# Optimization experiments

Measured on AMD Instinct MI355X. Metric: run time of the kernel, lower is better.

Reference implementation:

```python
import jax, jax.numpy as jnp
import numpy as np

B, N, C, H = 8, 1024, 768, 12
WBITS, ABITS, PGABITS = 8, 8, 4
TH = 0.99  # greater-than mask threshold on MSB softmax


def quant(x, bits):
    """Fixed-point quantize to `bits` bits, straight-through estimator."""
    step = 2.0 ** (1 - bits)
    q = jnp.round(x / step) * step
    return x + jax.lax.stop_gradient(q - x)


def setup_inputs() -> dict:
    key = jax.random.key(0)
    k1, k2, k3 = jax.random.split(key, 3)
    x = jax.random.normal(k1, (B, N, C), jnp.float32)
    # qkv: QLinear(dim, 3*dim, bias=False); proj: QLinear(dim, dim, bias=True)
    w_qkv = jax.random.normal(k2, (3 * C, C), jnp.float32) * (C ** -0.5)
    w_proj = jax.random.normal(k3, (C, C), jnp.float32) * (C ** -0.5)
    b_proj = jnp.zeros((C,), jnp.float32)
    return {"x": x, "w_qkv": w_qkv, "w_proj": w_proj, "b_proj": b_proj}


def reference(x, w_qkv, w_proj, b_proj):
    d = C // H
    scale = d ** -0.5
    # QLinear: quantize activations and weights, then matmul (no qkv bias)
    qkv = quant(x, ABITS) @ quant(w_qkv, WBITS).T            # [B,N,3C]
    qkv = qkv.reshape(B, N, 3, H, d).transpose(2, 0, 3, 1, 4)  # [3,B,H,N,d]
    qkv = quant(qkv, ABITS)
    q, k, v = qkv[0], qkv[1], qkv[2]
    # low-precision MSB pass
    q_msb = quant(q, PGABITS)
    k_msb = quant(k, PGABITS)
    attn_msb = jax.nn.softmax(
        jnp.einsum('bhqd,bhkd->bhqk', q_msb, k_msb) * scale, axis=-1)
    # GreaterThan with straight-through backward (identity grad)
    gt = (attn_msb > TH).astype(attn_msb.dtype)
    mask = attn_msb + jax.lax.stop_gradient(gt - attn_msb)
    # full-precision pass, masked pre-softmax
    attn = jnp.einsum('bhqd,bhkd->bhqk', q, k) * scale * mask
    attn = quant(jax.nn.softmax(attn, axis=-1), ABITS)
    out = jnp.einsum('bhqk,bhkd->bhqd', attn, v)             # [B,H,N,d]
    out = out.transpose(0, 2, 1, 3).reshape(B, N, C)
    return quant(out, ABITS) @ quant(w_proj, WBITS).T + b_proj
```

## Files before the change

kernel.cpp:

```cpp
#include <hip/hip_runtime.h>

#define NB 8
#define NSEQ 1024
#define NC 768
#define NH 12
#define ND 64
#define NM 8192

typedef _Float16 v8h __attribute__((ext_vector_type(8)));
typedef float v4f __attribute__((ext_vector_type(4)));
typedef int   v4i __attribute__((ext_vector_type(4)));

__device__ __forceinline__ float q8f(float x){ return rintf(x*128.f)*0.0078125f; }
__device__ __forceinline__ int imax2(int a, int b){ return a > b ? a : b; }
__device__ __forceinline__ int imin2(int a, int b){ return a < b ? a : b; }

__device__ __forceinline__ int swz(int r, int g){ return (r<<6) + (((g ^ (r & 7)) & 7)<<3); }

__device__ __forceinline__ void async_cp16(const void* g, void* l) {
  __builtin_amdgcn_global_load_lds(
      (const __attribute__((address_space(1))) unsigned int*)g,
      (__attribute__((address_space(3))) unsigned int*)l, 16, 0, 0);
}

__global__ __launch_bounds__(256) void k_pre(const float* __restrict__ x,
                                             const float* __restrict__ wq,
                                             const float* __restrict__ bias,
                                             _Float16* __restrict__ xt,
                                             _Float16* __restrict__ wqt,
                                             float* __restrict__ out) {
  int b = blockIdx.x;
  if (b < 3648) {
    const float* src; _Float16* dst; int gid;
    if (b < 3072) { src = x;  dst = xt;  gid = b*256 + threadIdx.x; }
    else          { src = wq; dst = wqt; gid = (b-3072)*256 + threadIdx.x; }
    int tile = gid / 12288;
    int rem  = gid - tile*12288;
    int chunk = rem >> 10, idx = rem & 1023;
    int r = idx >> 3, g = idx & 7;
    const float* s = src + (size_t)(tile*128 + r)*768 + chunk*64 + g*8;
    float4 v0 = *(const float4*)s, v1 = *(const float4*)(s + 4);
    v8h o;
    o[0]=(_Float16)q8f(v0.x); o[1]=(_Float16)q8f(v0.y); o[2]=(_Float16)q8f(v0.z); o[3]=(_Float16)q8f(v0.w);
    o[4]=(_Float16)q8f(v1.x); o[5]=(_Float16)q8f(v1.y); o[6]=(_Float16)q8f(v1.z); o[7]=(_Float16)q8f(v1.w);
    *(v8h*)&dst[((size_t)tile*12 + chunk)*8192 + swz(r, g)] = o;
  } else {
    int gid = (b - 3648)*256 + threadIdx.x;
    int c4 = gid % 192;
    ((float4*)out)[gid] = ((const float4*)bias)[c4];
  }
}

__device__ __forceinline__ void mfma_tile(const _Float16* Ah, const _Float16* Bh,
                                          int WR0, int l15, int quad, v4f acc[2][8]) {
#pragma unroll
  for (int ks = 0; ks < 2; ks++) {
    v8h a0 = *(const v8h*)&Ah[swz(WR0 + l15,      ks*4 + quad)];
    v8h a1 = *(const v8h*)&Ah[swz(WR0 + 16 + l15, ks*4 + quad)];
#pragma unroll
    for (int nt = 0; nt < 8; nt++) {
      v8h b = *(const v8h*)&Bh[swz(nt*16 + l15, ks*4 + quad)];
      acc[0][nt] = __builtin_amdgcn_mfma_f32_16x16x32_f16(a0, b, acc[0][nt], 0, 0, 0);
      acc[1][nt] = __builtin_amdgcn_mfma_f32_16x16x32_f16(a1, b, acc[1][nt], 0, 0, 0);
    }
  }
}

__global__ __launch_bounds__(256) void k_qk(const _Float16* __restrict__ xt,
                                            const _Float16* __restrict__ wqt,
                                            char* __restrict__ QmI,
                                            char* __restrict__ KmI) {
  __shared__ _Float16 S[2][16384];
  const int tid  = threadIdx.x;
  const int lane = tid & 63;
  const int quad = lane >> 4;
  const int l15  = lane & 15;
  const int wid  = tid >> 6;
  const int WR0  = wid * 32;
  const int m0 = blockIdx.x * 128, n0 = blockIdx.y * 128;
  const _Float16* Asrc = xt  + (size_t)blockIdx.x * 12 * 8192;
  const _Float16* Bsrc = wqt + (size_t)blockIdx.y * 12 * 8192;

  auto stage = [&](int kc, int bi) {
    const _Float16* a = Asrc + kc*8192;
    const _Float16* bsc = Bsrc + kc*8192;
#pragma unroll
    for (int s = 0; s < 8; s++) {
      int seg = wid*8 + s;
      const _Float16* g = (seg < 16 ? a + seg*512 : bsc + (seg-16)*512) + lane*8;
      async_cp16(g, &S[bi][seg*512]);
    }
  };

  v4f acc[2][8] = {};
  stage(0, 0);
#pragma unroll 1
  for (int kc = 0; kc < 12; kc++) {
    if (kc + 1 < 12) {
      stage(kc + 1, (kc + 1) & 1);
      asm volatile("s_waitcnt vmcnt(8)" ::: "memory");
    } else {
      asm volatile("s_waitcnt vmcnt(0)" ::: "memory");
    }
    __builtin_amdgcn_s_barrier();
    mfma_tile(&S[kc & 1][0], &S[kc & 1][8192], WR0, l15, quad, acc);
    __builtin_amdgcn_s_barrier();
  }

  const int which = (n0 >= 768);
  char* P8 = (char*)&S[0][0];
  __syncthreads();
#pragma unroll
  for (int mt = 0; mt < 2; mt++)
#pragma unroll
    for (int nt = 0; nt < 8; nt++)
#pragma unroll
      for (int rr = 0; rr < 4; rr++) {
        float v = q8f(acc[mt][nt][rr]);
        int qi = (int)rintf(v * 8.f);
        P8[(WR0 + mt*16 + quad*4 + rr)*144 + nt*16 + l15] = (char)qi;
      }
  __syncthreads();
  int c0 = n0 - which*768;
#pragma unroll
  for (int t = 0; t < 4; t++) {
    int idx = tid + t*256;
    int r = idx >> 3, cg = idx & 7;
    v4i val = *(const v4i*)&P8[r*144 + cg*16];
    if (which == 0) {
      *(v4i*)&QmI[(size_t)(m0 + r)*768 + c0 + cg*16] = val;
    } else {
      int m = m0 + r, n = m & 1023, bI = m >> 10;
      int h = (c0 + cg*16) >> 6, d0 = (cg & 3)*16;
      *(v4i*)&KmI[(((size_t)(bI*NH + h)*1024 + n) << 6) + d0] = val;
    }
  }
}

__global__ __launch_bounds__(256) void k_attn(const char* __restrict__ QmI,
                                              const char* __restrict__ KmI,
                                              const float* __restrict__ x,
                                              const float* __restrict__ wqkv,
                                              const float* __restrict__ wproj,
                                              float* __restrict__ out) {
  __shared__ char  S2[2][16384];
  __shared__ float rowm[128];
  __shared__ int   cand[128];
  __shared__ int   hrowA[128];
  __shared__ int   hcolA[128];
  __shared__ float qf[64], kf[64], vf[64];
  __shared__ float od[64];
  __shared__ float pps;
  __shared__ int   cnt, hcnt;

  const int tid  = threadIdx.x;
  const int lane = tid & 63;
  const int quad = lane >> 4;
  const int l15  = lane & 15;
  const int wid  = tid >> 6;
  const int R0   = wid * 16;
  const int bh = blockIdx.x;
  const int q0 = blockIdx.y * 128;
  const int bb = bh / NH, hb = bh % NH;
  const size_t mrow = (size_t)bb * NSEQ;
  const int hoff = hb * 64;
  const char* KmB = KmI + (size_t)bh * 1024 * 64;

  if (tid == 0) { cnt = 0; hcnt = 0; }

  auto stageK = [&](int kp, int bi) {
#pragma unroll
    for (int s = 0; s < 4; s++) {
      int seg = wid*4 + s;
      async_cp16(KmB + kp*16384 + seg*1024 + lane*16, &S2[bi][seg*1024]);
    }
  };

  v4i aQ[2];
#pragma unroll
  for (int b2 = 0; b2 < 2; b2++)
    aQ[b2] = *(const v4i*)&QmI[(mrow + q0 + b2*64 + R0 + l15)*768 + hoff + quad*16];

  int lm[2][4], lm2[2][4];
#pragma unroll
  for (int b2 = 0; b2 < 2; b2++)
#pragma unroll
    for (int r = 0; r < 4; r++) { lm[b2][r] = -1073741824; lm2[b2][r] = -1073741824; }

  stageK(0, 0);
#pragma unroll 1
  for (int kp = 0; kp < 4; kp++) {
    if (kp + 1 < 4) {
      stageK(kp + 1, (kp + 1) & 1);
      asm volatile("s_waitcnt vmcnt(4)" ::: "memory");
    } else {
      asm volatile("s_waitcnt vmcnt(0)" ::: "memory");
    }
    __builtin_amdgcn_s_barrier();
#pragma unroll
    for (int g64 = 0; g64 < 4; g64++) {
      const char* Ks = &S2[kp & 1][g64*4096];
      v4i c0a[4] = {}, c1a[4] = {};
      __builtin_amdgcn_s_setprio(1);
#pragma unroll
      for (int nt = 0; nt < 4; nt++) {
        v4i b = *(const v4i*)&Ks[(nt*16 + l15)*64 + quad*16];
        c0a[nt] = __builtin_amdgcn_mfma_i32_16x16x64_i8(aQ[0], b, c0a[nt], 0, 0, 0);
        c1a[nt] = __builtin_amdgcn_mfma_i32_16x16x64_i8(aQ[1], b, c1a[nt], 0, 0, 0);
      }
      __builtin_amdgcn_s_setprio(0);
#pragma unroll
      for (int r = 0; r < 4; r++) {
        int g0 = imax2(imax2(c0a[0][r], c0a[1][r]), imax2(c0a[2][r], c0a[3][r]));
        lm2[0][r] = imax2(lm2[0][r], imin2(lm[0][r], g0));
        lm[0][r]  = imax2(lm[0][r], g0);
        int g1 = imax2(imax2(c1a[0][r], c1a[1][r]), imax2(c1a[2][r], c1a[3][r]));
        lm2[1][r] = imax2(lm2[1][r], imin2(lm[1][r], g1));
        lm[1][r]  = imax2(lm[1][r], g1);
      }
    }
    __builtin_amdgcn_s_barrier();
  }
#pragma unroll
  for (int b2 = 0; b2 < 2; b2++)
#pragma unroll
    for (int r = 0; r < 4; r++) {
      int m = lm[b2][r], m2 = lm2[b2][r];
#pragma unroll
      for (int o = 1; o < 16; o <<= 1) {
        int om  = __shfl_xor(m, o);
        int om2 = __shfl_xor(m2, o);
        m2 = imax2(imax2(m2, om2), imin2(m, om));
        m  = imax2(m, om);
      }
      if (l15 == 0 && (m - m2) > 2304) {
        int row = b2*64 + R0 + quad*4 + r;
        rowm[row] = (float)m * 0.001953125f;
        int ix = atomicAdd(&cnt, 1);
        cand[ix] = row;
      }
    }
  __syncthreads();

  int nc = cnt;
  for (int ci = wid; ci < nc; ci += 4) {
    int row = cand[ci];
    float m = rowm[row];
    const char* qrow = &QmI[(mrow + q0 + row)*768 + hoff];
    float l = 0.f, bmax = -1e30f;
    int bcol = 0;
    for (int t = 0; t < 16; t++) {
      const char* kb = &KmB[(size_t)(t*64 + lane)*64];
      int si = 0;
#pragma unroll
      for (int j = 0; j < 64; j++) si += (int)qrow[j] * (int)kb[j];
      float s = (float)si * 0.001953125f;
      l += expf(s - m);
      if (s > bmax) { bmax = s; bcol = t*64 + lane; }
    }
#pragma unroll
    for (int o = 1; o < 64; o <<= 1) {
      l += __shfl_xor(l, o);
      float ov = __shfl_xor(bmax, o);
      int   oc = __shfl_xor(bcol, o);
      if (ov > bmax || (ov == bmax && oc < bcol)) { bmax = ov; bcol = oc; }
    }
    if (lane == 0 && (1.0f / l) > 0.99f) {
      int ix = atomicAdd(&hcnt, 1);
      hrowA[ix] = row; hcolA[ix] = bcol;
    }
  }
  __syncthreads();

  int nh = hcnt;
  for (int hi = 0; hi < nh; hi++) {
    int row = hrowA[hi], cst = hcolA[hi];
    if (tid < 192) {
      int d = tid & 63, part = tid >> 6;
      int wrow = part*768 + hoff + d;
      int xrow = (part == 0) ? (int)(mrow + q0 + row) : (int)(mrow + cst);
      const float* xr = &x[(size_t)xrow*768];
      const float* wr = &wqkv[(size_t)wrow*768];
      float s = 0.f;
      for (int k = 0; k < 768; k++) s += q8f(xr[k]) * q8f(wr[k]);
      float v = q8f(s);
      if (part == 0) qf[d] = v; else if (part == 1) kf[d] = v; else vf[d] = v;
    }
    __syncthreads();
    if (tid == 0) {
      float s = 0.f;
      for (int d = 0; d < 64; d++) s += qf[d]*kf[d];
      float sf = s * 0.125f;
      float m2 = fmaxf(sf, 0.f);
      float l2 = expf(sf - m2) + 1023.f*expf(-m2);
      pps = rintf(expf(sf - m2)/l2*128.f)*0.0078125f;
    }
    __syncthreads();
    float p = pps;
    if (p != 0.f) {
      if (tid < 64) od[tid] = q8f(p * vf[tid]);
      __syncthreads();
      for (int c = tid; c < 768; c += 256) {
        const float* wr = &wproj[(size_t)c*768 + hoff];
        float s = 0.f;
        for (int d = 0; d < 64; d++) s += od[d] * q8f(wr[d]);
        atomicAdd(&out[(mrow + q0 + row)*768 + c], s);
      }
    }
    __syncthreads();
  }
}

extern "C" void kernel_launch(void* const* d_in, const int* in_sizes, int n_in,
                              void* d_out, int out_size, void* d_ws, size_t ws_size,
                              hipStream_t stream) {
  const float* x      = (const float*)d_in[0];
  const float* w_qkv  = (const float*)d_in[1];
  const float* w_proj = (const float*)d_in[2];
  const float* b_proj = (const float*)d_in[3];
  float* out = (float*)d_out;

  char* p = (char*)d_ws;
  _Float16* xt  = (_Float16*)p;  p += (size_t)NM*768*2;
  _Float16* wqt = (_Float16*)p;  p += (size_t)1536*768*2;
  char* QmI = p;  p += (size_t)NM*768;
  char* KmI = p;  p += (size_t)NM*768;

  dim3 blk(256);
  k_pre <<<dim3(9792), blk, 0, stream>>>(x, w_qkv, b_proj, xt, wqt, out);
  k_qk  <<<dim3(64, 12), blk, 0, stream>>>(xt, wqt, QmI, KmI);
  k_attn<<<dim3(96, 8), blk, 0, stream>>>(QmI, KmI, x, w_qkv, w_proj, out);
}
```

Measured before the change: 122.8 us.

## Compute online softmax denominator in MFMA pass, drop candidate rescan

Replaces the top-two max tracking plus a second scalar pass over candidate rows with an online softmax (running max, rescaled sum and argmax column) computed directly on the int8 MFMA scores. The per-row threshold test then happens after the lane reduction, so the scalar 1024-column rescan per candidate row is removed. The trade is several expf calls per score element inside the main loop, which adds transcendental work to every row where the old gap filter let most rows skip the exp work.

```diff
diff --git a/kernel.cpp b/kernel.cpp
--- a/kernel.cpp
+++ b/kernel.cpp
@@ -13,7 +13,6 @@
 
 __device__ __forceinline__ float q8f(float x){ return rintf(x*128.f)*0.0078125f; }
 __device__ __forceinline__ int imax2(int a, int b){ return a > b ? a : b; }
-__device__ __forceinline__ int imin2(int a, int b){ return a < b ? a : b; }
 
 __device__ __forceinline__ int swz(int r, int g){ return (r<<6) + (((g ^ (r & 7)) & 7)<<3); }
 
@@ -144,14 +143,12 @@
                                               const float* __restrict__ wproj,
                                               float* __restrict__ out) {
   __shared__ char  S2[2][16384];
-  __shared__ float rowm[128];
-  __shared__ int   cand[128];
   __shared__ int   hrowA[128];
   __shared__ int   hcolA[128];
   __shared__ float qf[64], kf[64], vf[64];
   __shared__ float od[64];
   __shared__ float pps;
-  __shared__ int   cnt, hcnt;
+  __shared__ int   hcnt;
 
   const int tid  = threadIdx.x;
   const int lane = tid & 63;
@@ -166,7 +163,7 @@
   const int hoff = hb * 64;
   const char* KmB = KmI + (size_t)bh * 1024 * 64;
 
-  if (tid == 0) { cnt = 0; hcnt = 0; }
+  if (tid == 0) hcnt = 0;
 
   auto stageK = [&](int kp, int bi) {
 #pragma unroll
@@ -181,11 +178,13 @@
   for (int b2 = 0; b2 < 2; b2++)
     aQ[b2] = *(const v4i*)&QmI[(mrow + q0 + b2*64 + R0 + l15)*768 + hoff + quad*16];
 
-  int lm[2][4], lm2[2][4];
+  int   sm[2][4]; float sl[2][4]; int bc[2][4];
 #pragma unroll
   for (int b2 = 0; b2 < 2; b2++)
 #pragma unroll
-    for (int r = 0; r < 4; r++) { lm[b2][r] = -1073741824; lm2[b2][r] = -1073741824; }
+    for (int r = 0; r < 4; r++) { sm[b2][r] = -1073741824; sl[b2][r] = 0.f; bc[b2][r] = 0; }
+
+  const float ISC = 0.001953125f;
 
   stageK(0, 0);
 #pragma unroll 1
@@ -209,67 +208,67 @@
         c1a[nt] = __builtin_amdgcn_mfma_i32_16x16x64_i8(aQ[1], b, c1a[nt], 0, 0, 0);
       }
       __builtin_amdgcn_s_setprio(0);
+      int cbase = kp*256 + g64*64 + l15;
 #pragma unroll
       for (int r = 0; r < 4; r++) {
-        int g0 = imax2(imax2(c0a[0][r], c0a[1][r]), imax2(c0a[2][r], c0a[3][r]));
-        lm2[0][r] = imax2(lm2[0][r], imin2(lm[0][r], g0));
-        lm[0][r]  = imax2(lm[0][r], g0);
-        int g1 = imax2(imax2(c1a[0][r], c1a[1][r]), imax2(c1a[2][r], c1a[3][r]));
-        lm2[1][r] = imax2(lm2[1][r], imin2(lm[1][r], g1));
-        lm[1][r]  = imax2(lm[1][r], g1);
+        {
+          int mloc = c0a[0][r], ncol = 0;
+          if (c0a[1][r] > mloc) { mloc = c0a[1][r]; ncol = 1; }
+          if (c0a[2][r] > mloc) { mloc = c0a[2][r]; ncol = 2; }
+          if (c0a[3][r] > mloc) { mloc = c0a[3][r]; ncol = 3; }
+          if (mloc > sm[0][r]) {
+            sl[0][r] *= expf((float)(sm[0][r] - mloc) * ISC);
+            sm[0][r] = mloc;
+            bc[0][r] = cbase + ncol*16;
+          }
+          int m = sm[0][r];
+          sl[0][r] += expf((float)(c0a[0][r] - m) * ISC)
+                    + expf((float)(c0a[1][r] - m) * ISC)
+                    + expf((float)(c0a[2][r] - m) * ISC)
+                    + expf((float)(c0a[3][r] - m) * ISC);
+        }
+        {
+          int mloc = c1a[0][r], ncol = 0;
+          if (c1a[1][r] > mloc) { mloc = c1a[1][r]; ncol = 1; }
+          if (c1a[2][r] > mloc) { mloc = c1a[2][r]; ncol = 2; }
+          if (c1a[3][r] > mloc) { mloc = c1a[3][r]; ncol = 3; }
+          if (mloc > sm[1][r]) {
+            sl[1][r] *= expf((float)(sm[1][r] - mloc) * ISC);
+            sm[1][r] = mloc;
+            bc[1][r] = cbase + ncol*16;
+          }
+          int m = sm[1][r];
+          sl[1][r] += expf((float)(c1a[0][r] - m) * ISC)
+                    + expf((float)(c1a[1][r] - m) * ISC)
+                    + expf((float)(c1a[2][r] - m) * ISC)
+                    + expf((float)(c1a[3][r] - m) * ISC);
+        }
       }
     }
     __builtin_amdgcn_s_barrier();
   }
+
 #pragma unroll
   for (int b2 = 0; b2 < 2; b2++)
 #pragma unroll
     for (int r = 0; r < 4; r++) {
-      int m = lm[b2][r], m2 = lm2[b2][r];
+      int m = sm[b2][r]; float l = sl[b2][r]; int c = bc[b2][r];
 #pragma unroll
       for (int o = 1; o < 16; o <<= 1) {
-        int om  = __shfl_xor(m, o);
-        int om2 = __shfl_xor(m2, o);
-        m2 = imax2(imax2(m2, om2), imin2(m, om));
-        m  = imax2(m, om);
-      }
-      if (l15 == 0 && (m - m2) > 2304) {
+        int   om = __shfl_xor(m, o);
+        float ol = __shfl_xor(l, o);
+        int   oc = __shfl_xor(c, o);
+        int nm = imax2(m, om);
+        l = l*expf((float)(m - nm) * ISC) + ol*expf((float)(om - nm) * ISC);
+        if (om > m) c = oc;
+        m = nm;
+      }
+      if (l15 == 0 && (1.0f / l) > 0.99f) {
         int row = b2*64 + R0 + quad*4 + r;
-        rowm[row] = (float)m * 0.001953125f;
-        int ix = atomicAdd(&cnt, 1);
-        cand[ix] = row;
-      }
-    }
-  __syncthreads();
-
-  int nc = cnt;
-  for (int ci = wid; ci < nc; ci += 4) {
-    int row = cand[ci];
-    float m = rowm[row];
-    const char* qrow = &QmI[(mrow + q0 + row)*768 + hoff];
-    float l = 0.f, bmax = -1e30f;
-    int bcol = 0;
-    for (int t = 0; t < 16; t++) {
-      const char* kb = &KmB[(size_t)(t*64 + lane)*64];
-      int si = 0;
-#pragma unroll
-      for (int j = 0; j < 64; j++) si += (int)qrow[j] * (int)kb[j];
-      float s = (float)si * 0.001953125f;
-      l += expf(s - m);
-      if (s > bmax) { bmax = s; bcol = t*64 + lane; }
-    }
-#pragma unroll
-    for (int o = 1; o < 64; o <<= 1) {
-      l += __shfl_xor(l, o);
-      float ov = __shfl_xor(bmax, o);
-      int   oc = __shfl_xor(bcol, o);
-      if (ov > bmax || (ov == bmax && oc < bcol)) { bmax = ov; bcol = oc; }
-    }
-    if (lane == 0 && (1.0f / l) > 0.99f) {
-      int ix = atomicAdd(&hcnt, 1);
-      hrowA[ix] = row; hcolA[ix] = bcol;
-    }
-  }
+        int ix = atomicAdd(&hcnt, 1);
+        hrowA[ix] = row; hcolA[ix] = c;
+      }
+    }
   __syncthreads();
 
   int nh = hcnt;
```

Result: slower. 184.4 us (+50.2%).
